# Optimization experiments

Hardware: AMD Instinct MI355X
Metric: run time of the kernel (lower is better)

Reference implementation:

```python
import jax, jax.numpy as jnp
import numpy as np

B, L, D, T = 32, 512, 1024, 256
MAX_MENTION_LEN = 10
NEG_INF = float('-inf')


def _static_bounds_and_keep():
    # Full (start, end) grid, flattened row-major like torch's .view(-1, 2)
    s = np.repeat(np.arange(L), L)
    e = np.tile(np.arange(L), L)
    bounds = np.stack([s, e], axis=-1)            # [L*L, 2]
    keep = (e - s) <= MAX_MENTION_LEN             # static per-position mask
    idx = np.nonzero(keep)[0]
    return jnp.asarray(bounds[keep], jnp.int32), jnp.asarray(idx, jnp.int32)


def setup_inputs() -> dict:
    key = jax.random.key(0)
    k0, k1, k2 = jax.random.split(key, 3)
    text_encodings = jax.random.normal(k0, (B, L, D), dtype=jnp.float32)
    mask_ctxt = jnp.ones((B, L), dtype=jnp.int32)
    # word -> wordpiece mapping: [start, end_exclusive); values kept in [1, L)
    tokens_mapping = jax.random.randint(k1, (B, T, 2), 1, L).astype(jnp.int32)
    W = jax.random.normal(k2, (D, 3), dtype=jnp.float32) * 0.02
    b = jnp.zeros((3,), dtype=jnp.float32)
    return {"text_encodings": text_encodings, "mask_ctxt": mask_ctxt,
            "tokens_mapping": tokens_mapping, "W": W, "b": b}


def reference(text_encodings, mask_ctxt, tokens_mapping, W, b):
    # per-token start / end / mention logits
    logits = jnp.einsum('bld,dk->blk', text_encodings, W) + b  # [B, L, 3]
    valid_tok = (mask_ctxt == 1)
    start_lp = jnp.where(valid_tok, logits[:, :, 0], NEG_INF)
    end_lp = jnp.where(valid_tok, logits[:, :, 1], NEG_INF)
    mention_lp = jnp.where(valid_tok, logits[:, :, 2], NEG_INF)

    # scores[b, s, e] = start[b, s] + end[b, e] + sum_{i=s..e} mention[b, i]
    scores = start_lp[:, :, None] + end_lp[:, None, :]          # [B, L, L]
    csum = jnp.cumsum(mention_lp, axis=1)                        # [B, L]
    csum_prev = jnp.concatenate(
        [jnp.zeros((csum.shape[0], 1), csum.dtype), csum[:, :-1]], axis=1)
    scores = scores + (csum[:, None, :] - csum_prev[:, :, None])

    # mention_sizes > 0  <=>  e >= s
    pos = jnp.arange(L)
    size_ok = pos[None, :, None] <= pos[None, None, :]           # [1, L, L]

    # token-boundary masks (scatter 1 at word starts / ends, zero col 0)
    bidx = jnp.arange(tokens_mapping.shape[0])[:, None]
    ts = jnp.zeros(mask_ctxt.shape, jnp.int32).at[bidx, tokens_mapping[:, :, 0]].set(1)
    ts = ts.at[:, 0].set(0)
    te = jnp.zeros(mask_ctxt.shape, jnp.int32).at[bidx, tokens_mapping[:, :, 1] - 1].set(1)
    te = te.at[:, 0].set(0)
    vse = ts[:, :, None] * te[:, None, :]                        # bmm outer product

    valid = size_ok & (mask_ctxt[:, :, None] > 0) & (vse > 0)
    scores = jnp.where(valid, scores, NEG_INF)

    scores_flat = scores.reshape(scores.shape[0], -1)            # [B, L*L]
    bounds_keep, keep_idx = _static_bounds_and_keep()
    out_scores = scores_flat[:, keep_idx]                        # [B, K]
    out_bounds = jnp.broadcast_to(bounds_keep[None],
                                  (scores.shape[0],) + bounds_keep.shape)
    return out_scores, out_bounds
```

## Files before the change

### kernel.cpp

```cpp
#include <hip/hip_runtime.h>
#include <math.h>

#define BB 32
#define LL 512
#define DD 1024
#define TT 256
#define NK 136393
#define NK_LIN 131273
#define S_LIN 502
#define NEG_BIG  -3.0e38f
#define NEG_MASK -1.0e30f
#define P_TOT (BB * NK)
#define FILL_THREADS (P_TOT / 4)
#define FILL_BLOCKS ((FILL_THREADS + 255) / 256)
#define GEMV_BLOCKS (BB * LL / 4)

typedef float f4v __attribute__((ext_vector_type(4)));

__device__ __forceinline__ int off_s(int s) {
    return (s <= S_LIN) ? s * (s + 21) / 2 : NK_LIN + (s - S_LIN) * LL;
}

__global__ __launch_bounds__(256) void mega_kernel(
    const float* __restrict__ text, const float* __restrict__ W,
    const float* __restrict__ bias, const int* __restrict__ mask,
    float* __restrict__ out,
    float* __restrict__ slp, float* __restrict__ elp, float* __restrict__ mlp)
{
    if (blockIdx.x < FILL_BLOCKS) {
        const int i = blockIdx.x * 256 + threadIdx.x;
        if (i >= FILL_THREADS) return;
        const int idx = i * 4;

        f4v neg = {NEG_BIG, NEG_BIG, NEG_BIG, NEG_BIG};
        *(f4v*)(out + idx) = neg;

        int k = idx - (idx / NK) * NK;
        int s, e;
        if (k >= NK_LIN) {
            const int r = k - NK_LIN;
            s = S_LIN + (r >> 9);
            e = r & 511;
        } else {
            float f = sqrtf(8.0f * (float)k + 441.0f);
            s = (int)((f - 21.0f) * 0.5f);
            if (s < 0) s = 0;
            if (s > 501) s = 501;
            while ((s + 1) * (s + 22) / 2 <= k) ++s;
            while (s * (s + 21) / 2 > k) --s;
            e = k - s * (s + 21) / 2;
        }
        float bs[8];
#pragma unroll
        for (int j = 0; j < 4; ++j) {
            bs[2 * j] = (float)s; bs[2 * j + 1] = (float)e;
            ++e;
            const int rowlen = (s <= S_LIN) ? (s + 11) : LL;
            if (e >= rowlen) { e = 0; if (++s >= LL) s = 0; }
        }
        f4v* bp = (f4v*)(out + (size_t)P_TOT + (size_t)2 * idx);
        f4v b0 = {bs[0], bs[1], bs[2], bs[3]};
        f4v b1 = {bs[4], bs[5], bs[6], bs[7]};
        bp[0] = b0; bp[1] = b1;
        return;
    }

    const int gb   = blockIdx.x - FILL_BLOCKS;
    const int wid  = threadIdx.x >> 6;
    const int lane = threadIdx.x & 63;
    const int row  = gb * 4 + wid;

    const f4v* t4 = (const f4v*)(text + (size_t)row * DD);
    const f4v* w4 = (const f4v*)W;
    float a0 = 0.f, a1 = 0.f, a2 = 0.f;
#pragma unroll
    for (int j = 0; j < 4; ++j) {
        const int fi = lane + j * 64;
        f4v v  = t4[fi];
        f4v w0 = w4[fi * 3 + 0];
        f4v w1 = w4[fi * 3 + 1];
        f4v w2 = w4[fi * 3 + 2];
        a0 += v.x * w0.x;  a1 += v.x * w0.y;  a2 += v.x * w0.z;
        a0 += v.y * w0.w;  a1 += v.y * w1.x;  a2 += v.y * w1.y;
        a0 += v.z * w1.z;  a1 += v.z * w1.w;  a2 += v.z * w2.x;
        a0 += v.w * w2.y;  a1 += v.w * w2.z;  a2 += v.w * w2.w;
    }
#pragma unroll
    for (int o = 32; o; o >>= 1) {
        a0 += __shfl_down(a0, o);
        a1 += __shfl_down(a1, o);
        a2 += __shfl_down(a2, o);
    }
    if (lane == 0) {
        const int m = mask[row];
        slp[row] = (m == 1) ? a0 + bias[0] : NEG_MASK;
        elp[row] = (m == 1) ? a1 + bias[1] : NEG_MASK;
        mlp[row] = (m == 1) ? a2 + bias[2] : NEG_MASK;
    }
}

__global__ __launch_bounds__(512) void scatter_kernel(
    const float* __restrict__ slp, const float* __restrict__ elp,
    const float* __restrict__ mlp, const int* __restrict__ mask,
    const int* __restrict__ tmap, float* __restrict__ out)
{
    const int b = blockIdx.x;
    const int t = threadIdx.x;
    __shared__ float sl[LL], el[LL], ml[LL];
    __shared__ unsigned char tsl[LL], tel[LL];

    tsl[t] = 0; tel[t] = 0;
    const int idx = b * LL + t;
    sl[t] = slp[idx]; el[t] = elp[idx]; ml[t] = mlp[idx];
    __syncthreads();
    if (t < TT) {
        int s0 = tmap[((size_t)b * TT + t) * 2 + 0];
        int e0 = tmap[((size_t)b * TT + t) * 2 + 1] - 1;
        s0 = min(max(s0, 0), LL - 1);
        e0 = min(max(e0, 0), LL - 1);
        tsl[s0] = 1;
        tel[e0] = 1;
    }
    __syncthreads();

    const int s = t;
    if (s > 0 && tsl[s] && mask[idx] == 1) {
        const size_t obase = (size_t)b * NK + off_s(s);
        const float sv = sl[s];
        const int emax = min(LL - 1, s + 10);
        float w = 0.f;
        for (int e = s; e <= emax; ++e) {
            w += ml[e];
            if (tel[e]) {
                float sc = sv + el[e] + w;
                if (sc < -1.0e29f) sc = NEG_BIG;
                out[obase + e] = sc;
            }
        }
    }
}

extern "C" void kernel_launch(void* const* d_in, const int* in_sizes, int n_in,
                              void* d_out, int out_size, void* d_ws, size_t ws_size,
                              hipStream_t stream) {
    const float* text = (const float*)d_in[0];
    const int*   mask = (const int*)d_in[1];
    const int*   tmap = (const int*)d_in[2];
    const float* W    = (const float*)d_in[3];
    const float* bias = (const float*)d_in[4];
    float* out = (float*)d_out;

    float* slp = (float*)d_ws;
    float* elp = slp + (size_t)BB * LL;
    float* mlp = elp + (size_t)BB * LL;

    mega_kernel<<<FILL_BLOCKS + GEMV_BLOCKS, 256, 0, stream>>>(
        text, W, bias, mask, out, slp, elp, mlp);
    scatter_kernel<<<BB, 512, 0, stream>>>(slp, elp, mlp, mask, tmap, out);
}
```

Before: 29.22 us.

## Fuse GEMV and scatter into one kernel with interleaved fill and bounds blocks

Merges the two launches into a single kernel. Each GEMV block now computes the logits for 64 rows plus a 10-row halo in shared memory, so it can write that window's scores directly without a workspace round trip or a second launch. Fill blocks write NEG_BIG only to the invalid lower-triangle slots, leaving valid slots to the GEMV blocks. Bounds blocks compute the (s,e) inversion once and write it for 16 batches, and the three block roles are interleaved across the grid with period 19. The cost is redundant GEMV work on the halo rows and per-block W loads into registers.

```diff
diff --git a/kernel.cpp b/kernel.cpp
--- a/kernel.cpp
+++ b/kernel.cpp
@@ -11,131 +11,205 @@
 #define NEG_BIG  -3.0e38f
 #define NEG_MASK -1.0e30f
 #define P_TOT (BB * NK)
-#define FILL_THREADS (P_TOT / 4)
-#define FILL_BLOCKS ((FILL_THREADS + 255) / 256)
-#define GEMV_BLOCKS (BB * LL / 4)
+#define SC4 (P_TOT / 4)
+#define GEMV_CNT 256
+#define MEMSET_CNT ((SC4 + 255) / 256)
+#define NP2 ((NK + 1) / 2)
+#define BND_PER_GRP ((NP2 + 255) / 256)
+#define BND_CNT (BND_PER_GRP * 2)
+#define PERIOD 19
+#define NPER 267
+#define GRID (PERIOD * NPER)
 
 typedef float f4v __attribute__((ext_vector_type(4)));
+typedef float f2v __attribute__((ext_vector_type(2)));
 
 __device__ __forceinline__ int off_s(int s) {
     return (s <= S_LIN) ? s * (s + 21) / 2 : NK_LIN + (s - S_LIN) * LL;
 }
-
-__global__ __launch_bounds__(256) void mega_kernel(
+__device__ __forceinline__ void invert(int k, int& s, int& e) {
+    if (k >= NK_LIN) {
+        const int r = k - NK_LIN;
+        s = S_LIN + (r >> 9);
+        e = r & 511;
+    } else {
+        float f = sqrtf(8.0f * (float)k + 441.0f);
+        s = (int)((f - 21.0f) * 0.5f);
+        if (s < 0) s = 0;
+        if (s > 501) s = 501;
+        while ((s + 1) * (s + 22) / 2 <= k) ++s;
+        while (s * (s + 21) / 2 > k) --s;
+        e = k - s * (s + 21) / 2;
+    }
+}
+
+#define FMA_ROW(vv, A0, A1, A2)                                          \
+    {                                                                    \
+        _Pragma("unroll")                                                \
+        for (int j = 0; j < 4; ++j) {                                    \
+            f4v v = vv[j];                                               \
+            f4v w0 = wr[j*3], w1 = wr[j*3+1], w2 = wr[j*3+2];            \
+            A0 += v.x * w0.x;  A1 += v.x * w0.y;  A2 += v.x * w0.z;      \
+            A0 += v.y * w0.w;  A1 += v.y * w1.x;  A2 += v.y * w1.y;      \
+            A0 += v.z * w1.z;  A1 += v.z * w1.w;  A2 += v.z * w2.x;      \
+            A0 += v.w * w2.y;  A1 += v.w * w2.z;  A2 += v.w * w2.w;      \
+        }                                                                \
+    }
+
+__global__ __launch_bounds__(256) void mega(
     const float* __restrict__ text, const float* __restrict__ W,
     const float* __restrict__ bias, const int* __restrict__ mask,
-    float* __restrict__ out,
-    float* __restrict__ slp, float* __restrict__ elp, float* __restrict__ mlp)
-{
-    if (blockIdx.x < FILL_BLOCKS) {
-        const int i = blockIdx.x * 256 + threadIdx.x;
-        if (i >= FILL_THREADS) return;
-        const int idx = i * 4;
-
-        f4v neg = {NEG_BIG, NEG_BIG, NEG_BIG, NEG_BIG};
-        *(f4v*)(out + idx) = neg;
-
-        int k = idx - (idx / NK) * NK;
-        int s, e;
-        if (k >= NK_LIN) {
-            const int r = k - NK_LIN;
-            s = S_LIN + (r >> 9);
-            e = r & 511;
-        } else {
-            float f = sqrtf(8.0f * (float)k + 441.0f);
-            s = (int)((f - 21.0f) * 0.5f);
-            if (s < 0) s = 0;
-            if (s > 501) s = 501;
-            while ((s + 1) * (s + 22) / 2 <= k) ++s;
-            while (s * (s + 21) / 2 > k) --s;
-            e = k - s * (s + 21) / 2;
-        }
-        float bs[8];
-#pragma unroll
-        for (int j = 0; j < 4; ++j) {
-            bs[2 * j] = (float)s; bs[2 * j + 1] = (float)e;
-            ++e;
-            const int rowlen = (s <= S_LIN) ? (s + 11) : LL;
-            if (e >= rowlen) { e = 0; if (++s >= LL) s = 0; }
-        }
-        f4v* bp = (f4v*)(out + (size_t)P_TOT + (size_t)2 * idx);
-        f4v b0 = {bs[0], bs[1], bs[2], bs[3]};
-        f4v b1 = {bs[4], bs[5], bs[6], bs[7]};
-        bp[0] = b0; bp[1] = b1;
-        return;
-    }
-
-    const int gb   = blockIdx.x - FILL_BLOCKS;
-    const int wid  = threadIdx.x >> 6;
-    const int lane = threadIdx.x & 63;
-    const int row  = gb * 4 + wid;
-
-    const f4v* t4 = (const f4v*)(text + (size_t)row * DD);
-    const f4v* w4 = (const f4v*)W;
-    float a0 = 0.f, a1 = 0.f, a2 = 0.f;
-#pragma unroll
-    for (int j = 0; j < 4; ++j) {
-        const int fi = lane + j * 64;
-        f4v v  = t4[fi];
-        f4v w0 = w4[fi * 3 + 0];
-        f4v w1 = w4[fi * 3 + 1];
-        f4v w2 = w4[fi * 3 + 2];
-        a0 += v.x * w0.x;  a1 += v.x * w0.y;  a2 += v.x * w0.z;
-        a0 += v.y * w0.w;  a1 += v.y * w1.x;  a2 += v.y * w1.y;
-        a0 += v.z * w1.z;  a1 += v.z * w1.w;  a2 += v.z * w2.x;
-        a0 += v.w * w2.y;  a1 += v.w * w2.z;  a2 += v.w * w2.w;
-    }
-#pragma unroll
-    for (int o = 32; o; o >>= 1) {
-        a0 += __shfl_down(a0, o);
-        a1 += __shfl_down(a1, o);
-        a2 += __shfl_down(a2, o);
-    }
-    if (lane == 0) {
-        const int m = mask[row];
-        slp[row] = (m == 1) ? a0 + bias[0] : NEG_MASK;
-        elp[row] = (m == 1) ? a1 + bias[1] : NEG_MASK;
-        mlp[row] = (m == 1) ? a2 + bias[2] : NEG_MASK;
-    }
-}
-
-__global__ __launch_bounds__(512) void scatter_kernel(
-    const float* __restrict__ slp, const float* __restrict__ elp,
-    const float* __restrict__ mlp, const int* __restrict__ mask,
     const int* __restrict__ tmap, float* __restrict__ out)
 {
-    const int b = blockIdx.x;
-    const int t = threadIdx.x;
-    __shared__ float sl[LL], el[LL], ml[LL];
-    __shared__ unsigned char tsl[LL], tel[LL];
-
-    tsl[t] = 0; tel[t] = 0;
-    const int idx = b * LL + t;
-    sl[t] = slp[idx]; el[t] = elp[idx]; ml[t] = mlp[idx];
-    __syncthreads();
-    if (t < TT) {
-        int s0 = tmap[((size_t)b * TT + t) * 2 + 0];
-        int e0 = tmap[((size_t)b * TT + t) * 2 + 1] - 1;
-        s0 = min(max(s0, 0), LL - 1);
-        e0 = min(max(e0, 0), LL - 1);
-        tsl[s0] = 1;
-        tel[e0] = 1;
-    }
-    __syncthreads();
-
-    const int s = t;
-    if (s > 0 && tsl[s] && mask[idx] == 1) {
-        const size_t obase = (size_t)b * NK + off_s(s);
-        const float sv = sl[s];
-        const int emax = min(LL - 1, s + 10);
-        float w = 0.f;
-        for (int e = s; e <= emax; ++e) {
-            w += ml[e];
-            if (tel[e]) {
-                float sc = sv + el[e] + w;
-                if (sc < -1.0e29f) sc = NEG_BIG;
-                out[obase + e] = sc;
-            }
+    const int id = blockIdx.x;
+    const int q  = id / PERIOD;
+    const int r  = id - q * PERIOD;
+    const int t  = threadIdx.x;
+
+    if (r == 0) {
+        if (q >= GEMV_CNT) return;
+        const int b    = q >> 3;
+        const int r0l  = (q & 7) << 6;
+        const int wlen = min(74, LL - r0l);
+        const int wid  = t >> 6, lane = t & 63;
+
+        __shared__ float sl[74], el[74], ml[74];
+        __shared__ unsigned char tsw[74], tew[74];
+
+        const f4v* w4 = (const f4v*)W;
+        f4v wr[12];
+#pragma unroll
+        for (int j = 0; j < 4; ++j) {
+            const int fi = lane + j * 64;
+            wr[j*3+0] = w4[fi*3+0]; wr[j*3+1] = w4[fi*3+1]; wr[j*3+2] = w4[fi*3+2];
+        }
+        const float b0 = bias[0], b1 = bias[1], b2 = bias[2];
+
+        int lr = wid;
+        f4v cv[4];
+        if (lr < wlen) {
+            const f4v* t4 = (const f4v*)(text + (size_t)(b * LL + r0l + lr) * DD);
+#pragma unroll
+            for (int j = 0; j < 4; ++j) cv[j] = t4[lane + j * 64];
+        }
+        while (lr < wlen) {
+            const int nxt = lr + 4;
+            f4v nv[4];
+            if (nxt < wlen) {
+                const f4v* t4 = (const f4v*)(text + (size_t)(b * LL + r0l + nxt) * DD);
+#pragma unroll
+                for (int j = 0; j < 4; ++j) nv[j] = t4[lane + j * 64];
+            }
+            float a0 = 0.f, a1 = 0.f, a2 = 0.f;
+            FMA_ROW(cv, a0, a1, a2);
+#pragma unroll
+            for (int o = 32; o; o >>= 1) {
+                a0 += __shfl_down(a0, o);
+                a1 += __shfl_down(a1, o);
+                a2 += __shfl_down(a2, o);
+            }
+            if (lane == 0) {
+                const int m = mask[b * LL + r0l + lr];
+                sl[lr] = (m == 1) ? a0 + b0 : NEG_MASK;
+                el[lr] = (m == 1) ? a1 + b1 : NEG_MASK;
+                ml[lr] = (m == 1) ? a2 + b2 : NEG_MASK;
+            }
+#pragma unroll
+            for (int j = 0; j < 4; ++j) cv[j] = nv[j];
+            lr = nxt;
+        }
+
+        if (t < 74) { tsw[t] = 0; tew[t] = 0; }
+        __syncthreads();
+        {
+            int s0 = tmap[((size_t)b * TT + t) * 2 + 0];
+            int e0 = tmap[((size_t)b * TT + t) * 2 + 1] - 1;
+            s0 = min(max(s0, 0), LL - 1);
+            e0 = min(max(e0, 0), LL - 1);
+            if (s0 >= r0l && s0 < r0l + wlen) tsw[s0 - r0l] = 1;
+            if (e0 >= r0l && e0 < r0l + wlen) tew[e0 - r0l] = 1;
+        }
+        __syncthreads();
+
+        for (int it = t; it < 64 * 11; it += 256) {
+            const int s_loc = it / 11;
+            const int j     = it - s_loc * 11;
+            const int s     = r0l + s_loc;
+            const int e     = s + j;
+            if (e >= LL) continue;
+            const int e_loc = s_loc + j;
+            float v = NEG_BIG;
+            if (s > 0 && tsw[s_loc] && tew[e_loc]) {
+                float w = 0.f;
+                for (int l = s_loc; l <= e_loc; ++l) w += ml[l];
+                v = sl[s_loc] + el[e_loc] + w;
+                if (v < -1.0e29f) v = NEG_BIG;
+            }
+            out[(size_t)b * NK + off_s(s) + e] = v;
+        }
+        return;
+    }
+
+    if (r <= 16) {
+        const int m = q * 16 + (r - 1);
+        if (m >= MEMSET_CNT) return;
+        const int gid = m * 256 + t;
+        if (gid >= SC4) return;
+        const int p4 = gid * 4;
+        const int b  = p4 / NK;
+        const int k  = p4 - b * NK;
+        int s, e;
+        invert(k, s, e);
+        if (e + 3 < s) {
+            f4v neg = {NEG_BIG, NEG_BIG, NEG_BIG, NEG_BIG};
+            *(f4v*)(out + p4) = neg;
+        } else {
+            int rowlen = (s <= S_LIN) ? (s + 11) : LL;
+#pragma unroll
+            for (int kk = 0; kk < 4; ++kk) {
+                if (e < s) out[p4 + kk] = NEG_BIG;
+                ++e;
+                if (e >= rowlen) {
+                    e = 0; ++s;
+                    if (s >= LL) s = 0;
+                    rowlen = (s <= S_LIN) ? (s + 11) : LL;
+                }
+            }
+        }
+        return;
+    }
+
+    const int v = q * 2 + (r - 17);
+    if (v >= BND_CNT) return;
+    const int g  = (v >= BND_PER_GRP) ? 1 : 0;
+    const int c  = v - g * BND_PER_GRP;
+    const int pp = c * 256 + t;
+    if (pp >= NP2) return;
+    const int p = pp * 2;
+    int s, e;
+    invert(p, s, e);
+    int s1 = s, e1 = e + 1;
+    const int rowlen = (s <= S_LIN) ? (s + 11) : LL;
+    if (e1 >= rowlen) { e1 = 0; s1 = s + 1; if (s1 >= LL) s1 = 0; }
+    const bool has2 = (p + 1 < NK);
+    const float sf = (float)s, ef = (float)e, s1f = (float)s1, e1f = (float)e1;
+    float* bp = out + (size_t)P_TOT;
+#pragma unroll
+    for (int j = 0; j < 16; ++j) {
+        const int bb = g * 16 + j;
+        const size_t base = ((size_t)bb * NK + p) * 2;
+        if (has2) {
+            if ((bb & 1) == 0) {
+                f4v vv = {sf, ef, s1f, e1f};
+                *(f4v*)(bp + base) = vv;
+            } else {
+                f2v v0 = {sf, ef}, v1 = {s1f, e1f};
+                *(f2v*)(bp + base) = v0;
+                *(f2v*)(bp + base + 2) = v1;
+            }
+        } else {
+            f2v v0 = {sf, ef};
+            *(f2v*)(bp + base) = v0;
         }
     }
 }
@@ -150,11 +224,5 @@
     const float* bias = (const float*)d_in[4];
     float* out = (float*)d_out;
 
-    float* slp = (float*)d_ws;
-    float* elp = slp + (size_t)BB * LL;
-    float* mlp = elp + (size_t)BB * LL;
-
-    mega_kernel<<<FILL_BLOCKS + GEMV_BLOCKS, 256, 0, stream>>>(
-        text, W, bias, mask, out, slp, elp, mlp);
-    scatter_kernel<<<BB, 512, 0, stream>>>(slp, elp, mlp, mask, tmap, out);
-}
+    mega<<<GRID, 256, 0, stream>>>(text, W, bias, mask, tmap, out);
+}
```

New measurement: 37.69 us. 29.0% more time.
